# Performance work log

Measured on AMD Instinct MI355X. Metric: run time of the kernel, lower is better.

## Reference

```python
import jax, jax.numpy as jnp
import numpy as np

B, T, C, N = 2, 2048, 4096, 4096

def setup_inputs() -> dict:
    key = jax.random.key(0)
    k1, k2, k3, k4 = jax.random.split(key, 4)
    y = jax.random.normal(k1, (B, T, C), dtype=jnp.float32)
    # quantized weight: uint8 codes in [0,255], stored/used as float after upcast
    weight = jnp.round(jax.random.uniform(k2, (C, N), dtype=jnp.float32) * 255.0)
    rng = jax.random.uniform(k3, (1, 1, C), dtype=jnp.float32) * 0.01  # per-input-channel scale
    offset = jax.random.normal(k4, (C,), dtype=jnp.float32) * 0.01    # per-input-channel offset
    return {"y": y, "weight": weight, "rng": rng, "offset": offset}

def reference(y, weight, rng, offset):
    # yv = y.reshape(-1,C) @ offset -> [B,T,1] correction term
    yv = jnp.einsum('btc,c->bt', y, offset)[..., None]
    # (y * range) @ weight  (dequantized GEMM) + correction
    out = jnp.einsum('btc,cn->btn', y * rng, weight) + yv
    return out
```

## Files before the change

### kernel.cpp

```cpp
#include <hip/hip_runtime.h>

typedef unsigned short u16;
typedef unsigned int u32;
typedef unsigned char u8;
typedef signed char i8;

typedef int i32x4 __attribute__((ext_vector_type(4)));

__device__ inline void gld16(const i8* g, i8* l) {
    __builtin_amdgcn_global_load_lds((const __attribute__((address_space(1))) void*)g,
                                     (__attribute__((address_space(3))) void*)l,
                                     16, 0, 0);
}

__global__ __launch_bounds__(256) void prep_kernel(const float* __restrict__ y,
                                                   const float* __restrict__ rng,
                                                   const float* __restrict__ off,
                                                   const float* __restrict__ w,
                                                   uint4* __restrict__ qy,
                                                   uint4* __restrict__ wq,
                                                   float* __restrict__ sp,
                                                   float* __restrict__ tv) {
    __shared__ i8 tile[64][68];
    __shared__ float ra[4], rs1[4], rs2[4];
    const int tid = threadIdx.x;

    if (blockIdx.x < 4096) {
        const int row = blockIdx.x;
        const float* yr = y + (size_t)row * 4096;
        const int base = tid * 16;

        float ysr[16];
        float amax = 0.0f, s1 = 0.0f, s2 = 0.0f;
        #pragma unroll
        for (int ii = 0; ii < 4; ++ii) {
            float4 v = *(const float4*)&yr[base + ii * 4];
            float4 g = *(const float4*)&rng[base + ii * 4];
            float4 o = *(const float4*)&off[base + ii * 4];
            float p0 = v.x * g.x, p1 = v.y * g.y, p2 = v.z * g.z, p3 = v.w * g.w;
            ysr[ii * 4 + 0] = p0; ysr[ii * 4 + 1] = p1;
            ysr[ii * 4 + 2] = p2; ysr[ii * 4 + 3] = p3;
            s1 += p0 + p1 + p2 + p3;
            s2 += v.x * o.x + v.y * o.y + v.z * o.z + v.w * o.w;
            amax = fmaxf(amax, fmaxf(fmaxf(fabsf(p0), fabsf(p1)), fmaxf(fabsf(p2), fabsf(p3))));
        }
        #pragma unroll
        for (int d = 32; d > 0; d >>= 1) {
            amax = fmaxf(amax, __shfl_down(amax, d));
            s1 += __shfl_down(s1, d);
            s2 += __shfl_down(s2, d);
        }
        const int wv = tid >> 6;
        if ((tid & 63) == 0) { ra[wv] = amax; rs1[wv] = s1; rs2[wv] = s2; }
        __syncthreads();
        const float sm = fmaxf(fmaxf(ra[0], ra[1]), fmaxf(ra[2], ra[3]));
        const float inv = sm > 0.0f ? 127.0f / sm : 0.0f;

        u32 d[4];
        #pragma unroll
        for (int g = 0; g < 4; ++g) {
            u32 b0 = (u8)(i8)(int)rintf(ysr[g * 4 + 0] * inv);
            u32 b1 = (u8)(i8)(int)rintf(ysr[g * 4 + 1] * inv);
            u32 b2 = (u8)(i8)(int)rintf(ysr[g * 4 + 2] * inv);
            u32 b3 = (u8)(i8)(int)rintf(ysr[g * 4 + 3] * inv);
            d[g] = b0 | (b1 << 8) | (b2 << 16) | (b3 << 24);
        }
        const int j = (tid & 7) ^ (row & 7);
        qy[(size_t)row * 256 + (tid >> 3) * 8 + j] = make_uint4(d[0], d[1], d[2], d[3]);
        if (tid == 0) {
            sp[row] = sm / 127.0f;
            tv[row] = 128.0f * (rs1[0] + rs1[1] + rs1[2] + rs1[3])
                            + (rs2[0] + rs2[1] + rs2[2] + rs2[3]);
        }
    } else {
        const int bid = blockIdx.x - 4096;
        const int n0 = (bid & 63) * 64;
        const int k0 = (bid >> 6) * 64;
        const int c4 = tid & 15;
        const int r0 = tid >> 4;
        #pragma unroll
        for (int i = 0; i < 4; ++i) {
            int kk = r0 + i * 16;
            float4 v = *(const float4*)&w[(size_t)(k0 + kk) * 4096 + n0 + c4 * 4];
            u32 b0 = (u8)(i8)((int)v.x - 128);
            u32 b1 = (u8)(i8)((int)v.y - 128);
            u32 b2 = (u8)(i8)((int)v.z - 128);
            u32 b3 = (u8)(i8)((int)v.w - 128);
            *(u32*)&tile[kk][c4 * 4] = b0 | (b1 << 8) | (b2 << 16) | (b3 << 24);
        }
        __syncthreads();
        const int nl = tid >> 2;
        const int ci = tid & 3;
        const int l = ((k0 >> 4) & 7) + ci;
        const int j = l ^ ((n0 + nl) & 7);
        u32 d[4];
        #pragma unroll
        for (int g = 0; g < 4; ++g) {
            int kl = ci * 16 + g * 4;
            d[g] = (u32)(u8)tile[kl + 0][nl] | ((u32)(u8)tile[kl + 1][nl] << 8)
                 | ((u32)(u8)tile[kl + 2][nl] << 16) | ((u32)(u8)tile[kl + 3][nl] << 24);
        }
        wq[(size_t)(n0 + nl) * 256 + (k0 >> 7) * 8 + j] = make_uint4(d[0], d[1], d[2], d[3]);
    }
}

__global__ __launch_bounds__(512, 2) void gemm_kernel(const i8* __restrict__ qy,
                                                      const i8* __restrict__ wq,
                                                      const float* __restrict__ sp,
                                                      const float* __restrict__ tv,
                                                      float* __restrict__ out) {
    __shared__ i8 As[2][256 * 128];
    __shared__ i8 Bs[2][256 * 128];

    const int bid = blockIdx.x;
    const int xcd = bid & 7;
    const int jj = bid >> 3;
    const int bn = (xcd * 2 + (jj & 1)) * 256;
    const int bm = (jj >> 1) * 256;

    const int tid = (int)threadIdx.x;
    const int lane = tid & 63;
    const int wv = tid >> 6;
    const int wm = (wv >> 2) * 128;
    const int wn = (wv & 3) * 64;
    const int r = lane & 15;
    const int q = lane >> 4;
    const int col0 = (q ^ (r & 7)) << 4;

    const int offA0 = (wm + r) * 128 + col0;
    const int offB0 = (wn + r) * 128 + col0;
    const int offA1 = offA0 ^ 64;
    const int offB1 = offB0 ^ 64;

    const int rsub = lane >> 3;
    const int jsub = lane & 7;
    const i8* aP0 = qy + (size_t)(bm + wv * 8 + rsub) * 4096 + jsub * 16;
    const i8* bP0 = wq + (size_t)(bn + (wv >> 2) * 64 + (wv & 3) * 8 + rsub) * 4096 + jsub * 16;
    const int lAo = wv * 1024 + lane * 16;
    const int lBo = (wv >> 2) * 8192 + (wv & 3) * 1024 + lane * 16;

    size_t koff = 0;

#define STAGE_A(WB, H) do {                                                   \
        gld16(aP0 + koff + (size_t)((H) * 64) * 4096,       &As[WB][lAo + (H) * 8192]);          \
        gld16(aP0 + koff + (size_t)((H) * 64 + 128) * 4096, &As[WB][lAo + (H) * 8192 + 16384]);  \
    } while (0)
#define STAGE_B(WB, H) do {                                                   \
        gld16(bP0 + koff + (size_t)((H) * 32) * 4096,       &Bs[WB][lBo + (H) * 4096]);          \
        gld16(bP0 + koff + (size_t)((H) * 32 + 128) * 4096, &Bs[WB][lBo + (H) * 4096 + 16384]);  \
    } while (0)

    i32x4 acc[8][4] = {};
    i32x4 a[4][2], b[4][2];

    STAGE_A(0, 0); STAGE_B(0, 0); STAGE_B(0, 1);
    __builtin_amdgcn_sched_barrier(0);
    STAGE_A(0, 1);
    koff = 128;
    asm volatile("s_waitcnt vmcnt(2)" ::: "memory");
    __builtin_amdgcn_s_barrier();

#define RD_A4(RB, MB)                                                         \
    _Pragma("unroll")                                                         \
    for (int mi = 0; mi < 4; ++mi) {                                          \
        a[mi][0] = *(const i32x4*)&As[RB][offA0 + (MB + mi) * 2048];          \
        a[mi][1] = *(const i32x4*)&As[RB][offA1 + (MB + mi) * 2048];          \
    }
#define RD_B4(RB)                                                             \
    _Pragma("unroll")                                                         \
    for (int ni = 0; ni < 4; ++ni) {                                          \
        b[ni][0] = *(const i32x4*)&Bs[RB][offB0 + ni * 2048];                 \
        b[ni][1] = *(const i32x4*)&Bs[RB][offB1 + ni * 2048];                 \
    }
#define MM32(MB)                                                              \
    _Pragma("unroll")                                                         \
    for (int mi = 0; mi < 4; ++mi) {                                          \
        _Pragma("unroll")                                                     \
        for (int ni = 0; ni < 4; ++ni) {                                      \
            acc[MB + mi][ni] = __builtin_amdgcn_mfma_i32_16x16x64_i8(         \
                a[mi][0], b[ni][0], acc[MB + mi][ni], 0, 0, 0);               \
            acc[MB + mi][ni] = __builtin_amdgcn_mfma_i32_16x16x64_i8(         \
                a[mi][1], b[ni][1], acc[MB + mi][ni], 0, 0, 0);               \
        }                                                                     \
    }

#define KTILE(RB, WB, PF)                                                     \
    do {                                                                      \
                          \
        RD_A4(RB, 0);                                                         \
        RD_B4(RB);                                                            \
        if (PF) { STAGE_A(WB, 0); STAGE_B(WB, 0); }                           \
        asm volatile("s_waitcnt lgkmcnt(0)" ::: "memory");                    \
        __builtin_amdgcn_sched_barrier(0);                                    \
        __builtin_amdgcn_s_setprio(1); MM32(0); __builtin_amdgcn_s_setprio(0); \
        if (PF) asm volatile("s_waitcnt vmcnt(4)" ::: "memory");   \
        else    asm volatile("s_waitcnt vmcnt(0)" ::: "memory");              \
        __builtin_amdgcn_s_barrier();                                         \
                    \
        RD_A4(RB, 4);                                                         \
        if (PF) { STAGE_B(WB, 1); __builtin_amdgcn_sched_barrier(0); STAGE_A(WB, 1); } \
        asm volatile("s_waitcnt lgkmcnt(0)" ::: "memory");                    \
        __builtin_amdgcn_sched_barrier(0);                                    \
        __builtin_amdgcn_s_setprio(1); MM32(4); __builtin_amdgcn_s_setprio(0); \
        if (PF) asm volatile("s_waitcnt vmcnt(2)" ::: "memory");   \
        else    asm volatile("s_waitcnt vmcnt(0)" ::: "memory");              \
        __builtin_amdgcn_s_barrier();                                         \
        koff += 128;                                                          \
    } while (0)

    #pragma unroll 1
    for (int t = 0; t < 15; ++t) {
        KTILE(0, 1, 1);
        KTILE(1, 0, 1);
    }
    KTILE(0, 1, 1);
    KTILE(1, 0, 0);

#undef KTILE
#undef MM32
#undef RD_B4
#undef RD_A4
#undef STAGE_B
#undef STAGE_A

    #pragma unroll
    for (int mi = 0; mi < 8; ++mi) {
        #pragma unroll
        for (int rr = 0; rr < 4; ++rr) {
            const int gm = bm + wm + mi * 16 + q * 4 + rr;
            const float sc = sp[gm];
            const float tt = tv[gm];
            #pragma unroll
            for (int ni = 0; ni < 4; ++ni) {
                const int gn = bn + wn + ni * 16 + r;
                out[(size_t)gm * 4096 + gn] = sc * (float)acc[mi][ni][rr] + tt;
            }
        }
    }
}

extern "C" void kernel_launch(void* const* d_in, const int* in_sizes, int n_in,
                              void* d_out, int out_size, void* d_ws, size_t ws_size,
                              hipStream_t stream) {
    const float* y   = (const float*)d_in[0];
    const float* w   = (const float*)d_in[1];
    const float* rng = (const float*)d_in[2];
    const float* off = (const float*)d_in[3];
    float* out = (float*)d_out;

    i8* qy = (i8*)d_ws;
    i8* wq = qy + (size_t)4096 * 4096;
    float* sp = (float*)(wq + (size_t)4096 * 4096);
    float* tv = sp + 4096;

    prep_kernel<<<8192, 256, 0, stream>>>(y, rng, off, w, (uint4*)qy, (uint4*)wq, sp, tv);
    gemm_kernel<<<256, 512, 0, stream>>>(qy, wq, sp, tv, out);
}
```

Baseline: 238.5 us.

## Collapse K-tile pipeline to single barrier with upfront full-tile prefetch

Each K-tile now issues all global→LDS loads for the next buffer at the start, reads both A halves and B from LDS into separate registers, runs all 32 MFMAs together, then waits for all loads and syncs once. The earlier two-phase schedule with partial vmcnt waits and two barriers per tile is gone. This cuts barrier count and scheduling fragmentation, at the cost of more VGPRs (an extra A register set) and a coarser overlap between loads and compute.

```diff
diff --git a/kernel.cpp b/kernel.cpp
--- a/kernel.cpp
+++ b/kernel.cpp
@@ -149,22 +149,23 @@
         gld16(bP0 + koff + (size_t)((H) * 32) * 4096,       &Bs[WB][lBo + (H) * 4096]);          \
         gld16(bP0 + koff + (size_t)((H) * 32 + 128) * 4096, &Bs[WB][lBo + (H) * 4096 + 16384]);  \
     } while (0)
+#define STAGE_ALL(WB) do {                                                    \
+        STAGE_A(WB, 0); STAGE_A(WB, 1); STAGE_B(WB, 0); STAGE_B(WB, 1);       \
+    } while (0)
 
     i32x4 acc[8][4] = {};
-    i32x4 a[4][2], b[4][2];
-
-    STAGE_A(0, 0); STAGE_B(0, 0); STAGE_B(0, 1);
-    __builtin_amdgcn_sched_barrier(0);
-    STAGE_A(0, 1);
+    i32x4 a[4][2], aa[4][2], b[4][2];
+
+    STAGE_ALL(0);
     koff = 128;
-    asm volatile("s_waitcnt vmcnt(2)" ::: "memory");
+    asm volatile("s_waitcnt vmcnt(0)" ::: "memory");
     __builtin_amdgcn_s_barrier();
 
-#define RD_A4(RB, MB)                                                         \
+#define RD_A4(RB, MB, DST)                                                    \
     _Pragma("unroll")                                                         \
     for (int mi = 0; mi < 4; ++mi) {                                          \
-        a[mi][0] = *(const i32x4*)&As[RB][offA0 + (MB + mi) * 2048];          \
-        a[mi][1] = *(const i32x4*)&As[RB][offA1 + (MB + mi) * 2048];          \
+        DST[mi][0] = *(const i32x4*)&As[RB][offA0 + (MB + mi) * 2048];        \
+        DST[mi][1] = *(const i32x4*)&As[RB][offA1 + (MB + mi) * 2048];        \
     }
 #define RD_B4(RB)                                                             \
     _Pragma("unroll")                                                         \
@@ -172,38 +173,29 @@
         b[ni][0] = *(const i32x4*)&Bs[RB][offB0 + ni * 2048];                 \
         b[ni][1] = *(const i32x4*)&Bs[RB][offB1 + ni * 2048];                 \
     }
-#define MM32(MB)                                                              \
+#define MM32(MB, SRC)                                                         \
     _Pragma("unroll")                                                         \
     for (int mi = 0; mi < 4; ++mi) {                                          \
         _Pragma("unroll")                                                     \
         for (int ni = 0; ni < 4; ++ni) {                                      \
             acc[MB + mi][ni] = __builtin_amdgcn_mfma_i32_16x16x64_i8(         \
-                a[mi][0], b[ni][0], acc[MB + mi][ni], 0, 0, 0);               \
+                SRC[mi][0], b[ni][0], acc[MB + mi][ni], 0, 0, 0);             \
             acc[MB + mi][ni] = __builtin_amdgcn_mfma_i32_16x16x64_i8(         \
-                a[mi][1], b[ni][1], acc[MB + mi][ni], 0, 0, 0);               \
+                SRC[mi][1], b[ni][1], acc[MB + mi][ni], 0, 0, 0);             \
         }                                                                     \
     }
 
 #define KTILE(RB, WB, PF)                                                     \
     do {                                                                      \
-                          \
-        RD_A4(RB, 0);                                                         \
+        if (PF) { STAGE_ALL(WB); __builtin_amdgcn_sched_barrier(0); }         \
+        RD_A4(RB, 0, a);                                                      \
         RD_B4(RB);                                                            \
-        if (PF) { STAGE_A(WB, 0); STAGE_B(WB, 0); }                           \
-        asm volatile("s_waitcnt lgkmcnt(0)" ::: "memory");                    \
-        __builtin_amdgcn_sched_barrier(0);                                    \
-        __builtin_amdgcn_s_setprio(1); MM32(0); __builtin_amdgcn_s_setprio(0); \
-        if (PF) asm volatile("s_waitcnt vmcnt(4)" ::: "memory");   \
-        else    asm volatile("s_waitcnt vmcnt(0)" ::: "memory");              \
-        __builtin_amdgcn_s_barrier();                                         \
-                    \
-        RD_A4(RB, 4);                                                         \
-        if (PF) { STAGE_B(WB, 1); __builtin_amdgcn_sched_barrier(0); STAGE_A(WB, 1); } \
-        asm volatile("s_waitcnt lgkmcnt(0)" ::: "memory");                    \
-        __builtin_amdgcn_sched_barrier(0);                                    \
-        __builtin_amdgcn_s_setprio(1); MM32(4); __builtin_amdgcn_s_setprio(0); \
-        if (PF) asm volatile("s_waitcnt vmcnt(2)" ::: "memory");   \
-        else    asm volatile("s_waitcnt vmcnt(0)" ::: "memory");              \
+        RD_A4(RB, 4, aa);                                                     \
+        __builtin_amdgcn_s_setprio(1);                                        \
+        MM32(0, a);                                                           \
+        MM32(4, aa);                                                          \
+        __builtin_amdgcn_s_setprio(0);                                        \
+        asm volatile("s_waitcnt vmcnt(0)" ::: "memory");                      \
         __builtin_amdgcn_s_barrier();                                         \
         koff += 128;                                                          \
     } while (0)
@@ -220,6 +212,7 @@
 #undef MM32
 #undef RD_B4
 #undef RD_A4
+#undef STAGE_ALL
 #undef STAGE_B
 #undef STAGE_A
 
```

Measured after the change: 239.0 us. About the same (+0.2%).
